# Kernel tuning notes

Hardware: AMD Instinct MI355X
Metric: run time of the kernel (lower is better)

The kernel has to match this reference:

```python
import jax, jax.numpy as jnp
import numpy as np

B, S, D, H = 8, 512, 2048, 16
DOWN, UP, R = 512, 2048, 512
HD = D // H        # 128, used only in the additive scale
VHD = UP // H      # 128, content head dim / value head dim
BASE = 10000.0


def _rope_tables(head_dim):
    # Faithful to source: positions span arange(head_dim), NOT max_len.
    pos = jnp.arange(head_dim, dtype=jnp.float32)
    div = jnp.exp(jnp.arange(0, head_dim, 2, dtype=jnp.float32) * (-np.log(BASE) / head_dim))
    theta = jnp.outer(pos, div)          # [head_dim, head_dim//2]
    return jnp.sin(theta), jnp.cos(theta)


def _apply_rope(q, num_heads, head_dim):
    # q: [B, S, num_heads*head_dim] -> [B, num_heads, S, head_dim] with interleaved rotation
    b, s, _ = q.shape
    q = q.reshape(b, s, num_heads, head_dim).transpose(0, 2, 1, 3)
    sin, cos = _rope_tables(head_dim)
    sin = sin[:s][None, None]            # [1,1,S,head_dim//2]
    cos = cos[:s][None, None]
    q_ = q.reshape(b, num_heads, s, head_dim // 2, 2)
    q1, q2 = q_[..., 0], q_[..., 1]
    o1 = q1 * cos - q2 * sin
    o2 = q2 * cos + q1 * sin
    return jnp.stack([o1, o2], axis=-1).reshape(b, num_heads, s, head_dim)


def setup_inputs() -> dict:
    key = jax.random.key(0)
    ks = jax.random.split(key, 18)
    w = lambda k, shp: jax.random.normal(k, shp, jnp.float32) * 0.02
    return {
        "X":    jax.random.normal(ks[0], (B, S, D), jnp.float32),
        "Wdq":  w(ks[1], (D, DOWN)),      "bdq":  w(ks[2], (DOWN,)),
        "Wdkv": w(ks[3], (D, DOWN)),      "bdkv": w(ks[4], (DOWN,)),
        "Wuq":  w(ks[5], (DOWN, UP)),     "buq":  w(ks[6], (UP,)),
        "Wuk":  w(ks[7], (DOWN, UP)),     "buk":  w(ks[8], (UP,)),
        "Wuv":  w(ks[9], (DOWN, UP)),     "buv":  w(ks[10], (UP,)),
        "Wqr":  w(ks[11], (DOWN, R * H)), "bqr":  w(ks[12], (R * H,)),
        "Wkr":  w(ks[13], (D, R)),        "bkr":  w(ks[14], (R,)),
        "Wfc":  w(ks[15], (VHD * H, D)),  "bfc":  w(ks[16], (D,)),
    }


def reference(X, Wdq, bdq, Wdkv, bdkv, Wuq, buq, Wuk, buk, Wuv, buv,
              Wqr, bqr, Wkr, bkr, Wfc, bfc):
    b, s, _ = X.shape
    c_q = X @ Wdq + bdq                                  # [B,S,DOWN]
    c_kv = X @ Wdkv + bdkv                               # [B,S,DOWN]
    q_c = (c_q @ Wuq + buq).reshape(b, s, H, VHD).transpose(0, 2, 1, 3)   # [B,H,S,VHD]
    k_c = (c_kv @ Wuk + buk).reshape(b, s, H, VHD).transpose(0, 2, 1, 3)
    v_c = (c_kv @ Wuv + buv).reshape(b, s, H, VHD).transpose(0, 2, 1, 3)
    q_r = _apply_rope(c_q @ Wqr + bqr, H, R)             # [B,H,S,R]
    k_r = _apply_rope(X @ Wkr + bkr, 1, R)               # [B,1,S,R]
    q = jnp.concatenate([q_c, q_r], axis=-1)             # [B,H,S,VHD+R]
    k = jnp.concatenate([k_c, jnp.broadcast_to(k_r, (b, H, s, R))], axis=-1)
    scale = HD ** 0.5 + R ** 0.5                         # additive scale, as in source
    scores = jnp.einsum('bhqd,bhkd->bhqk', q, k) / scale
    attn = jax.nn.softmax(scores, axis=-1)               # dropout: eval mode (identity)
    o = jnp.einsum('bhqk,bhkd->bhqd', attn, v_c).transpose(0, 2, 1, 3).reshape(b, s, H * VHD)
    return o @ Wfc + bfc
```

## Files before the change

### kernel.cpp

```cpp
#include <hip/hip_runtime.h>
#include <hip/hip_bf16.h>
#include <stdint.h>

typedef unsigned short u16;
typedef short bf16x8 __attribute__((ext_vector_type(8)));
typedef float f32x4 __attribute__((ext_vector_type(4)));

__device__ __forceinline__ float us2f(u16 u) {
    union { unsigned int i; float f; } x;
    x.i = ((unsigned int)u) << 16;
    return x.f;
}

__device__ __forceinline__ u16 f2us(float f) {
    union { float f; unsigned int i; } x; x.f = f;
    unsigned int lsb = (x.i >> 16) & 1u;
    x.i += 0x7FFFu + lsb;
    return (u16)(x.i >> 16);
}

__device__ __forceinline__ void gl_lds16(const u16* g, u16* l) {
    __builtin_amdgcn_global_load_lds(
        (const __attribute__((address_space(1))) void*)(uintptr_t)(const void*)g,
        (__attribute__((address_space(3))) void*)(uintptr_t)(void*)l,
        16, 0, 0);
}

#define FLAG_ROPE2  1
#define FLAG_TRANS2 4
#define FLAG_F32OUT 8

struct GArgs {
    const u16 *A0, *B0, *B0r2;
    int K0;
    const float* bias;
    void* C; void* C2;
    int colSplit;
};

template <int LDA0, int LDB0, int LDC, int LDC2, int FLAGS>
__global__ __launch_bounds__(256)
void gemm_mfma(GArgs g)
{
    __shared__ u16 As[128 * 64];
    __shared__ u16 Bs[128 * 64];

    const int t    = threadIdx.x;
    const int lane = t & 63;
    const int w    = t >> 6;
    const int wm   = w >> 1, wn = w & 1;
    const int m0   = blockIdx.y * 128;
    const int n0   = blockIdx.x * 128;
    const bool r2  = (n0 >= g.colSplit);

    const int srow = t >> 3;
    const int sp   = t & 7;
    u16* dA = As + t * 8;
    u16* dB = Bs + t * 8;

    const int lr = lane & 15;
    const int jj = lane >> 4;

    f32x4 acc[4][4];
#pragma unroll
    for (int i = 0; i < 4; ++i)
#pragma unroll
        for (int j = 0; j < 4; ++j)
            acc[i][j] = (f32x4){0.f, 0.f, 0.f, 0.f};

    {
        const u16* A = g.A0;
        const u16* B = r2 ? g.B0r2 - (long)g.colSplit * LDB0 : g.B0;
        const u16* gA[4];
        const u16* gB[4];
#pragma unroll
        for (int r = 0; r < 4; ++r) {
            int row = r * 32 + srow;
            int gc  = (sp - row) & 7;
            gA[r] = A + (long)(m0 + row) * LDA0 + gc * 8;
            gB[r] = B + (long)(n0 + row) * LDB0 + gc * 8;
        }
        for (int kt = 0; kt < g.K0; kt += 64) {
#pragma unroll
            for (int r = 0; r < 4; ++r) {
                gl_lds16(gA[r], dA + r * 2048);
                gl_lds16(gB[r], dB + r * 2048);
                gA[r] += 64; gB[r] += 64;
            }
            __syncthreads();
#pragma unroll
            for (int s = 0; s < 2; ++s) {
                bf16x8 af[4], bfr[4];
#pragma unroll
                for (int mi = 0; mi < 4; ++mi) {
                    int row  = wm * 64 + mi * 16 + lr;
                    int slot = (s * 4 + jj + row) & 7;
                    af[mi] = *(const bf16x8*)&As[row * 64 + slot * 8];
                }
#pragma unroll
                for (int ni = 0; ni < 4; ++ni) {
                    int row  = wn * 64 + ni * 16 + lr;
                    int slot = (s * 4 + jj + row) & 7;
                    bfr[ni] = *(const bf16x8*)&Bs[row * 64 + slot * 8];
                }
#pragma unroll
                for (int mi = 0; mi < 4; ++mi)
#pragma unroll
                    for (int ni = 0; ni < 4; ++ni)
                        acc[mi][ni] = __builtin_amdgcn_mfma_f32_16x16x32_bf16(
                            af[mi], bfr[ni], acc[mi][ni], 0, 0, 0);
            }
            __syncthreads();
        }
    }

    const int eCol0 = n0 + wn * 64 + lr;
    const int eRow0 = m0 + wm * 64 + jj * 4;
    const bool oddc = lane & 1;

    if (g.bias) {
#pragma unroll
        for (int ni = 0; ni < 4; ++ni) {
            float bv = g.bias[eCol0 + ni * 16];
#pragma unroll
            for (int mi = 0; mi < 4; ++mi) {
                acc[mi][ni][0] += bv; acc[mi][ni][1] += bv;
                acc[mi][ni][2] += bv; acc[mi][ni][3] += bv;
            }
        }
    }

    if (!r2) {
#pragma unroll
        for (int mi = 0; mi < 4; ++mi)
#pragma unroll
            for (int ni = 0; ni < 4; ++ni) {
                int rowb = eRow0 + mi * 16;
                int colg = eCol0 + ni * 16;
                if (FLAGS & FLAG_F32OUT) {
                    float* cp = (float*)g.C;
#pragma unroll
                    for (int i = 0; i < 4; ++i)
                        cp[(long)(rowb + i) * LDC + colg] = acc[mi][ni][i];
                } else {
                    u16* cp = (u16*)g.C;
#pragma unroll
                    for (int i = 0; i < 4; ++i)
                        cp[(long)(rowb + i) * LDC + colg] = f2us(acc[mi][ni][i]);
                }
            }
    } else if (FLAGS & FLAG_ROPE2) {
        const float base_s = (float)(eRow0 & 511);
#pragma unroll
        for (int ni = 0; ni < 4; ++ni) {
            int col2 = eCol0 + ni * 16 - g.colSplit;
            int rp   = (col2 & 511) & ~1;
            float f  = __expf(-9.2103403719761836f * (float)rp * (1.0f / 512.0f));
            float s1, c1, s16, c16, sb, cb;
            __sincosf(f, &s1, &c1);
            __sincosf(16.0f * f, &s16, &c16);
            __sincosf(base_s * f, &sb, &cb);
            float cm = cb, sm = sb;
#pragma unroll
            for (int mi = 0; mi < 4; ++mi) {
                f32x4 v = acc[mi][ni];
                float cr = cm, sr = sm;
#pragma unroll
                for (int i = 0; i < 4; ++i) {
                    float other = __shfl_xor(v[i], 1, 64);
                    v[i] = oddc ? (v[i] * cr + other * sr)
                                : (v[i] * cr - other * sr);
                    float cn = cr * c1 - sr * s1;
                    sr = sr * c1 + cr * s1; cr = cn;
                }
                int rowb = eRow0 + mi * 16;
                u16* cp = (u16*)g.C2;
#pragma unroll
                for (int i = 0; i < 4; ++i)
                    cp[(long)(rowb + i) * LDC2 + col2] = f2us(v[i]);
                float cn = cm * c16 - sm * s16;
                sm = sm * c16 + cm * s16; cm = cn;
            }
        }
    } else {
#pragma unroll
        for (int mi = 0; mi < 4; ++mi)
#pragma unroll
            for (int ni = 0; ni < 4; ++ni) {
                int rowb = eRow0 + mi * 16;
                int col2 = eCol0 + ni * 16 - g.colSplit;
                if (FLAGS & FLAG_TRANS2) {
                    u16* cp = (u16*)g.C2 + (long)col2 * LDC2 + rowb;
                    ushort4 o4;
                    o4.x = f2us(acc[mi][ni][0]); o4.y = f2us(acc[mi][ni][1]);
                    o4.z = f2us(acc[mi][ni][2]); o4.w = f2us(acc[mi][ni][3]);
                    *(ushort4*)cp = o4;
                } else {
                    u16* cp = (u16*)g.C2;
#pragma unroll
                    for (int i = 0; i < 4; ++i)
                        cp[(long)(rowb + i) * LDC2 + col2] = f2us(acc[mi][ni][i]);
                }
            }
    }
}

struct U2 { GArgs q; GArgs kv; };

__global__ __launch_bounds__(256)
void gemm_up2(U2 u)
{
    __shared__ u16 As[128 * 64];
    __shared__ u16 Bs[128 * 64];

    const int fl = blockIdx.x;
    const int gi = fl / 7, ri = fl - gi * 7;
    const bool isQ = ri < 5;
    const int idx  = isQ ? gi * 5 + ri : gi * 2 + (ri - 5);
    int m0, n0;
    if (isQ) { n0 = (idx % 80) * 128; m0 = (idx / 80) * 128; }
    else     { n0 = (idx & 31) * 128; m0 = (idx >> 5) * 128; }
    const GArgs g = isQ ? u.q : u.kv;
    const bool r2 = (n0 >= 2048);

    const int t    = threadIdx.x;
    const int lane = t & 63;
    const int w    = t >> 6;
    const int wm   = w >> 1, wn = w & 1;

    const int srow = t >> 3;
    const int sp   = t & 7;
    u16* dA = As + t * 8;
    u16* dB = Bs + t * 8;

    const int lr = lane & 15;
    const int jj = lane >> 4;

    f32x4 acc[4][4];
#pragma unroll
    for (int i = 0; i < 4; ++i)
#pragma unroll
        for (int j = 0; j < 4; ++j)
            acc[i][j] = (f32x4){0.f, 0.f, 0.f, 0.f};

    {
        const u16* A = g.A0;
        const u16* B = r2 ? g.B0r2 - 2048l * 512 : g.B0;
        const u16* gA[4];
        const u16* gB[4];
#pragma unroll
        for (int r = 0; r < 4; ++r) {
            int row = r * 32 + srow;
            int gc  = (sp - row) & 7;
            gA[r] = A + (long)(m0 + row) * 1536 + gc * 8;
            gB[r] = B + (long)(n0 + row) * 512 + gc * 8;
        }
#pragma unroll 1
        for (int kt = 0; kt < 512; kt += 64) {
#pragma unroll
            for (int r = 0; r < 4; ++r) {
                gl_lds16(gA[r], dA + r * 2048);
                gl_lds16(gB[r], dB + r * 2048);
                gA[r] += 64; gB[r] += 64;
            }
            __syncthreads();
#pragma unroll
            for (int s = 0; s < 2; ++s) {
                bf16x8 af[4], bfr[4];
#pragma unroll
                for (int mi = 0; mi < 4; ++mi) {
                    int row  = wm * 64 + mi * 16 + lr;
                    int slot = (s * 4 + jj + row) & 7;
                    af[mi] = *(const bf16x8*)&As[row * 64 + slot * 8];
                }
#pragma unroll
                for (int ni = 0; ni < 4; ++ni) {
                    int row  = wn * 64 + ni * 16 + lr;
                    int slot = (s * 4 + jj + row) & 7;
                    bfr[ni] = *(const bf16x8*)&Bs[row * 64 + slot * 8];
                }
#pragma unroll
                for (int mi = 0; mi < 4; ++mi)
#pragma unroll
                    for (int ni = 0; ni < 4; ++ni)
                        acc[mi][ni] = __builtin_amdgcn_mfma_f32_16x16x32_bf16(
                            af[mi], bfr[ni], acc[mi][ni], 0, 0, 0);
            }
            __syncthreads();
        }
    }

    const int eCol0 = n0 + wn * 64 + lr;
    const int eRow0 = m0 + wm * 64 + jj * 4;
    const bool oddc = lane & 1;

#pragma unroll
    for (int ni = 0; ni < 4; ++ni) {
        float bv = g.bias[eCol0 + ni * 16];
#pragma unroll
        for (int mi = 0; mi < 4; ++mi) {
            acc[mi][ni][0] += bv; acc[mi][ni][1] += bv;
            acc[mi][ni][2] += bv; acc[mi][ni][3] += bv;
        }
    }

    if (!r2) {
        u16* cp = (u16*)g.C;
#pragma unroll
        for (int mi = 0; mi < 4; ++mi)
#pragma unroll
            for (int ni = 0; ni < 4; ++ni) {
                int rowb = eRow0 + mi * 16;
                int colg = eCol0 + ni * 16;
#pragma unroll
                for (int i = 0; i < 4; ++i)
                    cp[(long)(rowb + i) * 2048 + colg] = f2us(acc[mi][ni][i]);
            }
    } else if (isQ) {
        const float base_s = (float)(eRow0 & 511);
#pragma unroll
        for (int ni = 0; ni < 4; ++ni) {
            int col2 = eCol0 + ni * 16 - 2048;
            int rp   = (col2 & 511) & ~1;
            float f  = __expf(-9.2103403719761836f * (float)rp * (1.0f / 512.0f));
            float s1, c1, s16, c16, sb, cb;
            __sincosf(f, &s1, &c1);
            __sincosf(16.0f * f, &s16, &c16);
            __sincosf(base_s * f, &sb, &cb);
            float cm = cb, sm = sb;
#pragma unroll
            for (int mi = 0; mi < 4; ++mi) {
                f32x4 v = acc[mi][ni];
                float cr = cm, sr = sm;
#pragma unroll
                for (int i = 0; i < 4; ++i) {
                    float other = __shfl_xor(v[i], 1, 64);
                    v[i] = oddc ? (v[i] * cr + other * sr)
                                : (v[i] * cr - other * sr);
                    float cn = cr * c1 - sr * s1;
                    sr = sr * c1 + cr * s1; cr = cn;
                }
                int rowb = eRow0 + mi * 16;
                u16* cp = (u16*)g.C2;
#pragma unroll
                for (int i = 0; i < 4; ++i)
                    cp[(long)(rowb + i) * 8192 + col2] = f2us(v[i]);
                float cn = cm * c16 - sm * s16;
                sm = sm * c16 + cm * s16; cm = cn;
            }
        }
    } else {
#pragma unroll
        for (int mi = 0; mi < 4; ++mi)
#pragma unroll
            for (int ni = 0; ni < 4; ++ni) {
                int rowb = eRow0 + mi * 16;
                int col2 = eCol0 + ni * 16 - 2048;
                u16* cp = (u16*)g.C2 + (long)col2 * 4096 + rowb;
                ushort4 o4;
                o4.x = f2us(acc[mi][ni][0]); o4.y = f2us(acc[mi][ni][1]);
                o4.z = f2us(acc[mi][ni][2]); o4.w = f2us(acc[mi][ni][3]);
                *(ushort4*)cp = o4;
            }
    }
}

__global__ __launch_bounds__(256, 2)
void attn_fused(const u16* __restrict__ qc, const u16* __restrict__ kc,
                const u16* __restrict__ qr, const u16* __restrict__ kr,
                const u16* __restrict__ vt, u16* __restrict__ o)
{
    __shared__ u16 As[128 * 64];
    __shared__ u16 Bs[128 * 64];
    __shared__ u16 Ps[128 * 136];
    __shared__ float l_sum[128];

    const int t    = threadIdx.x;
    const int lane = t & 63;
    const int w    = t >> 6;
    const int wm   = w >> 1, wn = w & 1;

    const int flat = blockIdx.x + (blockIdx.y << 2);
    const int xcd  = flat & 7;
    const int j    = flat >> 3;
    const int m0   = (j >> 4) * 128;
    const int z    = xcd * 16 + (j & 15);
    const int bb   = z >> 4, h = z & 15;

    if (t < 128) l_sum[t] = 0.f;

    const int srow = t >> 3;
    const int sp   = t & 7;
    u16* dA = As + t * 8;
    u16* dB = Bs + t * 8;
    int rrow[4], rgc[4];
#pragma unroll
    for (int r = 0; r < 4; ++r) {
        rrow[r] = r * 32 + srow;
        rgc[r]  = (sp - rrow[r]) & 7;
    }

    const int lr = lane & 15;
    const int jj = lane >> 4;

    const u16* gqc[4];
    const u16* gqr[4];
#pragma unroll
    for (int r = 0; r < 4; ++r) {
        gqc[r] = qc + (long)(bb * 512 + m0 + rrow[r]) * 2048 + h * 128 + rgc[r] * 8;
        gqr[r] = qr + (long)(bb * 512 + m0 + rrow[r]) * 8192 + h * 512 + rgc[r] * 8;
    }

    f32x4 acc_o[4][4];
#pragma unroll
    for (int i = 0; i < 4; ++i)
#pragma unroll
        for (int j2 = 0; j2 < 4; ++j2) acc_o[i][j2] = (f32x4){0.f, 0.f, 0.f, 0.f};

    const float scale = 1.0f / 33.941125496954285f;

    for (int nt = 0; nt < 4; ++nt) {
        const int n0k = nt * 128;

        f32x4 acc_s[4][4];
#pragma unroll
        for (int i = 0; i < 4; ++i)
#pragma unroll
            for (int j2 = 0; j2 < 4; ++j2) acc_s[i][j2] = (f32x4){0.f, 0.f, 0.f, 0.f};

        const u16* pa[4];
        const u16* pb[4];
#pragma unroll
        for (int r = 0; r < 4; ++r) {
            pa[r] = gqc[r];
            pb[r] = kc + (long)(bb * 512 + n0k + rrow[r]) * 2048 + h * 128 + rgc[r] * 8;
        }
        for (int seg = 0; seg < 2; ++seg) {
            int iters = seg == 0 ? 2 : 8;
            for (int kt = 0; kt < iters; ++kt) {
#pragma unroll
                for (int r = 0; r < 4; ++r) {
                    gl_lds16(pa[r], dA + r * 2048);
                    gl_lds16(pb[r], dB + r * 2048);
                    pa[r] += 64; pb[r] += 64;
                }
                __syncthreads();
#pragma unroll
                for (int s = 0; s < 2; ++s) {
                    bf16x8 af[4], bfr[4];
#pragma unroll
                    for (int mi = 0; mi < 4; ++mi) {
                        int row  = wm * 64 + mi * 16 + lr;
                        int slot = (s * 4 + jj + row) & 7;
                        af[mi] = *(const bf16x8*)&As[row * 64 + slot * 8];
                    }
#pragma unroll
                    for (int ni = 0; ni < 4; ++ni) {
                        int row  = wn * 64 + ni * 16 + lr;
                        int slot = (s * 4 + jj + row) & 7;
                        bfr[ni] = *(const bf16x8*)&Bs[row * 64 + slot * 8];
                    }
#pragma unroll
                    for (int mi = 0; mi < 4; ++mi)
#pragma unroll
                        for (int ni = 0; ni < 4; ++ni)
                            acc_s[mi][ni] = __builtin_amdgcn_mfma_f32_16x16x32_bf16(
                                af[mi], bfr[ni], acc_s[mi][ni], 0, 0, 0);
                }
                __syncthreads();
            }
            if (seg == 0) {
#pragma unroll
                for (int r = 0; r < 4; ++r) {
                    pa[r] = gqr[r];
                    pb[r] = kr + (long)(bb * 512 + n0k + rrow[r]) * 1536 + rgc[r] * 8;
                }
            }
        }

#pragma unroll
        for (int mi = 0; mi < 4; ++mi) {
            float rowpart[4] = {0.f, 0.f, 0.f, 0.f};
#pragma unroll
            for (int ni = 0; ni < 4; ++ni) {
                f32x4 v = acc_s[mi][ni];
                int colP = wn * 64 + ni * 16 + lr;
#pragma unroll
                for (int i = 0; i < 4; ++i) {
                    float e = __expf(v[i] * scale);
                    rowpart[i] += e;
                    int rowP = wm * 64 + mi * 16 + jj * 4 + i;
                    Ps[rowP * 136 + colP] = f2us(e);
                }
            }
#pragma unroll
            for (int i = 0; i < 4; ++i) {
                float s4 = rowpart[i];
                s4 += __shfl_xor(s4, 1, 64);
                s4 += __shfl_xor(s4, 2, 64);
                s4 += __shfl_xor(s4, 4, 64);
                s4 += __shfl_xor(s4, 8, 64);
                if ((lane & 15) == 0)
                    atomicAdd(&l_sum[wm * 64 + mi * 16 + jj * 4 + i], s4);
            }
        }

        const u16* pv[4];
#pragma unroll
        for (int r = 0; r < 4; ++r)
            pv[r] = vt + (long)(h * 128 + rrow[r]) * 4096 + bb * 512 + n0k + rgc[r] * 8;
        for (int kt = 0; kt < 2; ++kt) {
#pragma unroll
            for (int r = 0; r < 4; ++r) {
                gl_lds16(pv[r], dB + r * 2048);
                pv[r] += 64;
            }
            __syncthreads();
#pragma unroll
            for (int s = 0; s < 2; ++s) {
                bf16x8 af[4], bfr[4];
#pragma unroll
                for (int mi = 0; mi < 4; ++mi) {
                    int row = wm * 64 + mi * 16 + lr;
                    af[mi] = *(const bf16x8*)&Ps[row * 136 + kt * 64 + s * 32 + jj * 8];
                }
#pragma unroll
                for (int ni = 0; ni < 4; ++ni) {
                    int row  = wn * 64 + ni * 16 + lr;
                    int slot = (s * 4 + jj + row) & 7;
                    bfr[ni] = *(const bf16x8*)&Bs[row * 64 + slot * 8];
                }
#pragma unroll
                for (int mi = 0; mi < 4; ++mi)
#pragma unroll
                    for (int ni = 0; ni < 4; ++ni)
                        acc_o[mi][ni] = __builtin_amdgcn_mfma_f32_16x16x32_bf16(
                            af[mi], bfr[ni], acc_o[mi][ni], 0, 0, 0);
            }
            __syncthreads();
        }
    }

#pragma unroll
    for (int mi = 0; mi < 4; ++mi) {
#pragma unroll
        for (int i = 0; i < 4; ++i) {
            int row = wm * 64 + mi * 16 + jj * 4 + i;
            float linv = 1.0f / l_sum[row];
            long grow = (long)(bb * 512 + m0 + row) * 2048 + h * 128;
#pragma unroll
            for (int ni = 0; ni < 4; ++ni) {
                int colc = wn * 64 + ni * 16 + lr;
                o[grow + colc] = f2us(acc_o[mi][ni][i] * linv);
            }
        }
    }
}

__global__ __launch_bounds__(256)
void conv_f32_bf16(const float* __restrict__ in, u16* __restrict__ out)
{
    int i = blockIdx.x * 256 + threadIdx.x;
    float4 v = ((const float4*)in)[i];
    ushort4 o;
    o.x = f2us(v.x); o.y = f2us(v.y); o.z = f2us(v.z); o.w = f2us(v.w);
    ((ushort4*)out)[i] = o;
}

struct TCAll {
    const float *Wdq, *Wdkv, *Wkr, *Wuq, *Wuk, *Wuv, *Wqr, *Wfc;
    u16 *Wc1, *Wc2, *Wqr_t, *Wfc_t;
};

__global__ __launch_bounds__(256)
void tconv_all(TCAll a)
{
    __shared__ float tile[32][33];
    const int bid = blockIdx.x;
    const float* in; u16* out; int K, N, nx, ny;
    if (bid < 3072) {
        int z = bid >> 10, rem = bid & 1023;
        in = z == 0 ? a.Wdq : (z == 1 ? a.Wdkv : a.Wkr);
        out = a.Wc1 + z * 1048576;
        K = 2048; N = 512; nx = rem & 15; ny = rem >> 4;
    } else if (bid < 6144) {
        int l = bid - 3072, z = l >> 10, rem = l & 1023;
        in = z == 0 ? a.Wuq : (z == 1 ? a.Wuk : a.Wuv);
        out = a.Wc2 + z * 1048576;
        K = 512; N = 2048; nx = rem & 63; ny = rem >> 6;
    } else if (bid < 10240) {
        int l = bid - 6144;
        in = a.Wqr; out = a.Wqr_t;
        K = 512; N = 8192; nx = l & 255; ny = l >> 8;
    } else {
        int l = bid - 10240;
        in = a.Wfc; out = a.Wfc_t;
        K = 2048; N = 2048; nx = l & 63; ny = l >> 6;
    }
    const int n0 = nx * 32, k0 = ny * 32;
    const int c = threadIdx.x & 31, r0 = threadIdx.x >> 5;
#pragma unroll
    for (int j = 0; j < 4; ++j) {
        int r = r0 + j * 8;
        tile[r][c] = in[(long)(k0 + r) * N + n0 + c];
    }
    __syncthreads();
#pragma unroll
    for (int j = 0; j < 4; ++j) {
        int r = r0 + j * 8;
        out[(long)(n0 + r) * K + k0 + c] = f2us(tile[c][r]);
    }
}

struct BG {
    const float *bdq, *bdkv, *bkr, *buq, *bqr, *buk, *buv;
    float *biasD, *biasQ, *biasK;
};

__global__ __launch_bounds__(256)
void bias_gather(BG a)
{
    int i = blockIdx.x * 256 + threadIdx.x;
    if (i < 1536) {
        float v = i < 512 ? a.bdq[i] : (i < 1024 ? a.bdkv[i - 512] : a.bkr[i - 1024]);
        a.biasD[i] = v;
    } else if (i < 11776) {
        int j = i - 1536;
        a.biasQ[j] = j < 2048 ? a.buq[j] : a.bqr[j - 2048];
    } else {
        int j = i - 11776;
        a.biasK[j] = j < 2048 ? a.buk[j] : a.buv[j - 2048];
    }
}

extern "C" void kernel_launch(void* const* d_in, const int* in_sizes, int n_in,
                              void* d_out, int out_size, void* d_ws, size_t ws_size,
                              hipStream_t stream)
{
    (void)in_sizes; (void)n_in; (void)out_size; (void)ws_size;

    const float* X    = (const float*)d_in[0];
    const float* Wdq  = (const float*)d_in[1];  const float* bdq  = (const float*)d_in[2];
    const float* Wdkv = (const float*)d_in[3];  const float* bdkv = (const float*)d_in[4];
    const float* Wuq  = (const float*)d_in[5];  const float* buq  = (const float*)d_in[6];
    const float* Wuk  = (const float*)d_in[7];  const float* buk  = (const float*)d_in[8];
    const float* Wuv  = (const float*)d_in[9];  const float* buv  = (const float*)d_in[10];
    const float* Wqr  = (const float*)d_in[11]; const float* bqr  = (const float*)d_in[12];
    const float* Wkr  = (const float*)d_in[13]; const float* bkr  = (const float*)d_in[14];
    const float* Wfc  = (const float*)d_in[15]; const float* bfc  = (const float*)d_in[16];
    float* out = (float*)d_out;

    u16* ws = (u16*)d_ws;
    u16* Xb     = ws;
    u16* Wc1    = Xb   + 8388608;
    u16* Wc2    = Wc1  + 3145728;
    u16* Wqr_t  = Wc2  + 3145728;
    u16* Wfc_t  = Wqr_t + 4194304;
    u16* ckk    = Wfc_t + 4194304;
    u16* q_c    = ckk  + 6291456;
    u16* k_c    = q_c  + 8388608;
    u16* v_t    = k_c  + 8388608;
    u16* q_r    = v_t  + 8388608;
    u16* o      = q_r  + 33554432;
    float* biasD = (float*)(o + 8388608);
    float* biasQ = biasD + 1536;
    float* biasK = biasQ + 10240;

    dim3 blk(256, 1, 1);

    conv_f32_bf16<<<8192, blk, 0, stream>>>(X, Xb);
    {   TCAll a{Wdq, Wdkv, Wkr, Wuq, Wuk, Wuv, Wqr, Wfc,
                Wc1, Wc2, Wqr_t, Wfc_t};
        tconv_all<<<14336, blk, 0, stream>>>(a); }
    {   BG a{bdq, bdkv, bkr, buq, bqr, buk, buv, biasD, biasQ, biasK};
        bias_gather<<<62, blk, 0, stream>>>(a); }

    const int NOSPLIT = 1 << 30;

    {
        GArgs a{};
        a.A0 = Xb; a.B0 = Wc1; a.B0r2 = Wc1 + 2l * 1048576; a.K0 = 2048;
        a.bias = biasD; a.C = ckk; a.C2 = ckk + 1024;
        a.colSplit = 1024;
        gemm_mfma<2048, 2048, 1536, 1536, FLAG_ROPE2>
            <<<dim3(12, 32, 1), blk, 0, stream>>>(a);
    }
    {
        U2 u{};
        u.q.A0 = ckk; u.q.B0 = Wc2; u.q.B0r2 = Wqr_t; u.q.K0 = 512;
        u.q.bias = biasQ; u.q.C = q_c; u.q.C2 = q_r; u.q.colSplit = 2048;
        u.kv.A0 = ckk + 512; u.kv.B0 = Wc2 + 1048576;
        u.kv.B0r2 = Wc2 + 2l * 1048576; u.kv.K0 = 512;
        u.kv.bias = biasK; u.kv.C = k_c; u.kv.C2 = v_t; u.kv.colSplit = 2048;
        gemm_up2<<<3584, blk, 0, stream>>>(u);
    }

    attn_fused<<<dim3(4, 128, 1), blk, 0, stream>>>(
        q_c, k_c, q_r, ckk + 1024, v_t, o);

    {
        GArgs a{};
        a.A0 = o; a.B0 = Wfc_t; a.B0r2 = Wfc_t; a.K0 = 2048;
        a.bias = bfc; a.C = out; a.C2 = out;
        a.colSplit = NOSPLIT;
        gemm_mfma<2048, 2048, 2048, 1, FLAG_F32OUT>
            <<<dim3(16, 32, 1), blk, 0, stream>>>(a);
    }
}
```

Measured before the change: 417.6 us.

## Merge prep kernels, parallelize RoPE rotation terms, raise MFMA wave priority

Folds the X conversion, the weight transpose-conversion and the bias gather into one prep launch, which removes two kernel launches and the gaps between them. The RoPE epilogues now compute the per-row cos/sin factors from precomputed small tables rather than a serial recurrence, which shortens the dependency chain and lets each value be stored as soon as it is rotated. The fused GEMM also raises wave priority with s_setprio around its MFMA section. These are three unrelated tweaks, and each one's effect is likely small.

```diff
diff --git a/kernel.cpp b/kernel.cpp
--- a/kernel.cpp
+++ b/kernel.cpp
@@ -24,6 +24,24 @@
         (const __attribute__((address_space(1))) void*)(uintptr_t)(const void*)g,
         (__attribute__((address_space(3))) void*)(uintptr_t)(void*)l,
         16, 0, 0);
+}
+
+__device__ __forceinline__ void rope_cs(float f, float base_s,
+                                        float (&Cm)[4], float (&Sm)[4],
+                                        float (&ci)[4], float (&si)[4])
+{
+    float s1, c1, s16, c16, sb, cb;
+    __sincosf(f, &s1, &c1);
+    __sincosf(16.0f * f, &s16, &c16);
+    __sincosf(base_s * f, &sb, &cb);
+    ci[0] = 1.f; si[0] = 0.f;
+    ci[1] = c1;  si[1] = s1;
+    ci[2] = c1 * c1 - s1 * s1;          si[2] = 2.f * s1 * c1;
+    ci[3] = ci[2] * c1 - si[2] * s1;    si[3] = si[2] * c1 + ci[2] * s1;
+    Cm[0] = cb; Sm[0] = sb;
+    Cm[1] = cb * c16 - sb * s16;        Sm[1] = sb * c16 + cb * s16;
+    Cm[2] = Cm[1] * c16 - Sm[1] * s16;  Sm[2] = Sm[1] * c16 + Cm[1] * s16;
+    Cm[3] = Cm[2] * c16 - Sm[2] * s16;  Sm[3] = Sm[2] * c16 + Cm[2] * s16;
 }
 
 #define FLAG_ROPE2  1
@@ -156,30 +174,22 @@
             int col2 = eCol0 + ni * 16 - g.colSplit;
             int rp   = (col2 & 511) & ~1;
             float f  = __expf(-9.2103403719761836f * (float)rp * (1.0f / 512.0f));
-            float s1, c1, s16, c16, sb, cb;
-            __sincosf(f, &s1, &c1);
-            __sincosf(16.0f * f, &s16, &c16);
-            __sincosf(base_s * f, &sb, &cb);
-            float cm = cb, sm = sb;
+            float Cm[4], Sm[4], ci[4], si[4];
+            rope_cs(f, base_s, Cm, Sm, ci, si);
+            u16* cp = (u16*)g.C2;
 #pragma unroll
             for (int mi = 0; mi < 4; ++mi) {
                 f32x4 v = acc[mi][ni];
-                float cr = cm, sr = sm;
+                int rowb = eRow0 + mi * 16;
 #pragma unroll
                 for (int i = 0; i < 4; ++i) {
+                    float cr = Cm[mi] * ci[i] - Sm[mi] * si[i];
+                    float sr = Sm[mi] * ci[i] + Cm[mi] * si[i];
                     float other = __shfl_xor(v[i], 1, 64);
-                    v[i] = oddc ? (v[i] * cr + other * sr)
-                                : (v[i] * cr - other * sr);
-                    float cn = cr * c1 - sr * s1;
-                    sr = sr * c1 + cr * s1; cr = cn;
-                }
-                int rowb = eRow0 + mi * 16;
-                u16* cp = (u16*)g.C2;
-#pragma unroll
-                for (int i = 0; i < 4; ++i)
-                    cp[(long)(rowb + i) * LDC2 + col2] = f2us(v[i]);
-                float cn = cm * c16 - sm * s16;
-                sm = sm * c16 + cm * s16; cm = cn;
+                    float ov = oddc ? (v[i] * cr + other * sr)
+                                    : (v[i] * cr - other * sr);
+                    cp[(long)(rowb + i) * LDC2 + col2] = f2us(ov);
+                }
             }
         }
     } else {
@@ -264,6 +274,7 @@
                 gA[r] += 64; gB[r] += 64;
             }
             __syncthreads();
+            __builtin_amdgcn_s_setprio(1);
 #pragma unroll
             for (int s = 0; s < 2; ++s) {
                 bf16x8 af[4], bfr[4];
@@ -286,6 +297,7 @@
                         acc[mi][ni] = __builtin_amdgcn_mfma_f32_16x16x32_bf16(
                             af[mi], bfr[ni], acc[mi][ni], 0, 0, 0);
             }
+            __builtin_amdgcn_s_setprio(0);
             __syncthreads();
         }
     }
@@ -323,30 +335,22 @@
             int col2 = eCol0 + ni * 16 - 2048;
             int rp   = (col2 & 511) & ~1;
             float f  = __expf(-9.2103403719761836f * (float)rp * (1.0f / 512.0f));
-            float s1, c1, s16, c16, sb, cb;
-            __sincosf(f, &s1, &c1);
-            __sincosf(16.0f * f, &s16, &c16);
-            __sincosf(base_s * f, &sb, &cb);
-            float cm = cb, sm = sb;
+            float Cm[4], Sm[4], ci[4], si[4];
+            rope_cs(f, base_s, Cm, Sm, ci, si);
+            u16* cp = (u16*)g.C2;
 #pragma unroll
             for (int mi = 0; mi < 4; ++mi) {
                 f32x4 v = acc[mi][ni];
-                float cr = cm, sr = sm;
+                int rowb = eRow0 + mi * 16;
 #pragma unroll
                 for (int i = 0; i < 4; ++i) {
+                    float cr = Cm[mi] * ci[i] - Sm[mi] * si[i];
+                    float sr = Sm[mi] * ci[i] + Cm[mi] * si[i];
                     float other = __shfl_xor(v[i], 1, 64);
-                    v[i] = oddc ? (v[i] * cr + other * sr)
-                                : (v[i] * cr - other * sr);
-                    float cn = cr * c1 - sr * s1;
-                    sr = sr * c1 + cr * s1; cr = cn;
-                }
-                int rowb = eRow0 + mi * 16;
-                u16* cp = (u16*)g.C2;
-#pragma unroll
-                for (int i = 0; i < 4; ++i)
-                    cp[(long)(rowb + i) * 8192 + col2] = f2us(v[i]);
-                float cn = cm * c16 - sm * s16;
-                sm = sm * c16 + cm * s16; cm = cn;
+                    float ov = oddc ? (v[i] * cr + other * sr)
+                                    : (v[i] * cr - other * sr);
+                    cp[(long)(rowb + i) * 8192 + col2] = f2us(ov);
+                }
             }
         }
     } else {
@@ -557,43 +561,62 @@
     }
 }
 
-__global__ __launch_bounds__(256)
-void conv_f32_bf16(const float* __restrict__ in, u16* __restrict__ out)
-{
-    int i = blockIdx.x * 256 + threadIdx.x;
-    float4 v = ((const float4*)in)[i];
-    ushort4 o;
-    o.x = f2us(v.x); o.y = f2us(v.y); o.z = f2us(v.z); o.w = f2us(v.w);
-    ((ushort4*)out)[i] = o;
-}
-
-struct TCAll {
+struct Prep {
+    const float* X; u16* Xb;
     const float *Wdq, *Wdkv, *Wkr, *Wuq, *Wuk, *Wuv, *Wqr, *Wfc;
     u16 *Wc1, *Wc2, *Wqr_t, *Wfc_t;
+    const float *bdq, *bdkv, *bkr, *buq, *bqr, *buk, *buv;
+    float *biasD, *biasQ, *biasK;
 };
 
 __global__ __launch_bounds__(256)
-void tconv_all(TCAll a)
+void prep_all(Prep a)
 {
     __shared__ float tile[32][33];
     const int bid = blockIdx.x;
+
+    if (bid < 8192) {
+        int i = bid * 256 + threadIdx.x;
+        float4 v = ((const float4*)a.X)[i];
+        ushort4 o;
+        o.x = f2us(v.x); o.y = f2us(v.y); o.z = f2us(v.z); o.w = f2us(v.w);
+        ((ushort4*)a.Xb)[i] = o;
+        return;
+    }
+    if (bid >= 22528) {
+        int i = (bid - 22528) * 256 + threadIdx.x;
+        if (i < 1536) {
+            float v = i < 512 ? a.bdq[i]
+                              : (i < 1024 ? a.bdkv[i - 512] : a.bkr[i - 1024]);
+            a.biasD[i] = v;
+        } else if (i < 11776) {
+            int j = i - 1536;
+            a.biasQ[j] = j < 2048 ? a.buq[j] : a.bqr[j - 2048];
+        } else {
+            int j = i - 11776;
+            a.biasK[j] = j < 2048 ? a.buk[j] : a.buv[j - 2048];
+        }
+        return;
+    }
+
+    const int wb = bid - 8192;
     const float* in; u16* out; int K, N, nx, ny;
-    if (bid < 3072) {
-        int z = bid >> 10, rem = bid & 1023;
+    if (wb < 3072) {
+        int z = wb >> 10, rem = wb & 1023;
         in = z == 0 ? a.Wdq : (z == 1 ? a.Wdkv : a.Wkr);
         out = a.Wc1 + z * 1048576;
         K = 2048; N = 512; nx = rem & 15; ny = rem >> 4;
-    } else if (bid < 6144) {
-        int l = bid - 3072, z = l >> 10, rem = l & 1023;
+    } else if (wb < 6144) {
+        int l = wb - 3072, z = l >> 10, rem = l & 1023;
         in = z == 0 ? a.Wuq : (z == 1 ? a.Wuk : a.Wuv);
         out = a.Wc2 + z * 1048576;
         K = 512; N = 2048; nx = rem & 63; ny = rem >> 6;
-    } else if (bid < 10240) {
-        int l = bid - 6144;
+    } else if (wb < 10240) {
+        int l = wb - 6144;
         in = a.Wqr; out = a.Wqr_t;
         K = 512; N = 8192; nx = l & 255; ny = l >> 8;
     } else {
-        int l = bid - 10240;
+        int l = wb - 10240;
         in = a.Wfc; out = a.Wfc_t;
         K = 2048; N = 2048; nx = l & 63; ny = l >> 6;
     }
@@ -609,27 +632,6 @@
     for (int j = 0; j < 4; ++j) {
         int r = r0 + j * 8;
         out[(long)(n0 + r) * K + k0 + c] = f2us(tile[c][r]);
-    }
-}
-
-struct BG {
-    const float *bdq, *bdkv, *bkr, *buq, *bqr, *buk, *buv;
-    float *biasD, *biasQ, *biasK;
-};
-
-__global__ __launch_bounds__(256)
-void bias_gather(BG a)
-{
-    int i = blockIdx.x * 256 + threadIdx.x;
-    if (i < 1536) {
-        float v = i < 512 ? a.bdq[i] : (i < 1024 ? a.bdkv[i - 512] : a.bkr[i - 1024]);
-        a.biasD[i] = v;
-    } else if (i < 11776) {
-        int j = i - 1536;
-        a.biasQ[j] = j < 2048 ? a.buq[j] : a.bqr[j - 2048];
-    } else {
-        int j = i - 11776;
-        a.biasK[j] = j < 2048 ? a.buk[j] : a.buv[j - 2048];
     }
 }
 
@@ -668,12 +670,14 @@
 
     dim3 blk(256, 1, 1);
 
-    conv_f32_bf16<<<8192, blk, 0, stream>>>(X, Xb);
-    {   TCAll a{Wdq, Wdkv, Wkr, Wuq, Wuk, Wuv, Wqr, Wfc,
-                Wc1, Wc2, Wqr_t, Wfc_t};
-        tconv_all<<<14336, blk, 0, stream>>>(a); }
-    {   BG a{bdq, bdkv, bkr, buq, bqr, buk, buv, biasD, biasQ, biasK};
-        bias_gather<<<62, blk, 0, stream>>>(a); }
+    {
+        Prep a{X, Xb,
+               Wdq, Wdkv, Wkr, Wuq, Wuk, Wuv, Wqr, Wfc,
+               Wc1, Wc2, Wqr_t, Wfc_t,
+               bdq, bdkv, bkr, buq, bqr, buk, buv,
+               biasD, biasQ, biasK};
+        prep_all<<<22590, blk, 0, stream>>>(a);
+    }
 
     const int NOSPLIT = 1 << 30;
 
```

Result: no change. 415.9 us (-0.4%).
